# Performance work log

Measured on AMD Instinct MI355X. Metric: run time of the kernel, lower is better.

Reference implementation:

```python
import jax, jax.numpy as jnp
import numpy as np

STRIDE = 1
PADDING = 3
DILATION = 1


def setup_inputs() -> dict:
    key = jax.random.key(0)
    k1, k2 = jax.random.split(key)
    B, C, H, W = 8, 512, 64, 64
    G, K = 8, 7
    Ho, Wo = H // STRIDE, W // STRIDE
    x = jax.random.normal(k1, (B, C, H, W), dtype=jnp.float32)
    weight = jax.random.normal(k2, (B, G, K, K, Ho, Wo), dtype=jnp.float32)
    return {"x": x, "weight": weight}


def reference(x, weight):
    # x: [B, C, H, W]; weight: [B, G, K, K, Ho, Wo]
    B, C, H, W = x.shape
    _, G, K, _, Ho, Wo = weight.shape
    cpg = C // G  # channels per group
    # zero-pad spatial dims (matches CUDA boundary check)
    xp = jnp.pad(x, ((0, 0), (0, 0), (PADDING, PADDING), (PADDING, PADDING)))
    out = jnp.zeros((B, G, cpg, Ho, Wo), dtype=x.dtype)
    for kh in range(K):
        for kw in range(K):
            h0 = kh * DILATION
            w0 = kw * DILATION
            # strided window: input pixel h*stride - pad + kh*dil for each output h
            patch = xp[:, :,
                       h0:h0 + (Ho - 1) * STRIDE + 1:STRIDE,
                       w0:w0 + (Wo - 1) * STRIDE + 1:STRIDE]  # [B, C, Ho, Wo]
            wk = weight[:, :, kh, kw]  # [B, G, Ho, Wo]
            out = out + patch.reshape(B, G, cpg, Ho, Wo) * wk[:, :, None]
    return out.reshape(B, C, Ho, Wo)
```

## Files before the change

kernel.cpp:

```cpp
#include <hip/hip_runtime.h>


#define BB 8
#define CC 512
#define GG 8
#define CPG 64
#define HH 64
#define WW 64
#define HW (HH * WW)
#define KK 7
#define PAD 3

#define TILE_ROWS 16
#define CSPLIT 16
#define CHPC 4
#define LDS_ROWS (TILE_ROWS + KK - 1)
#define LDS_PITCH 72
#define CH_STRIDE (LDS_ROWS * LDS_PITCH)
#define PLANE_QUADS (LDS_ROWS * (LDS_PITCH / 4))
#define TOT_QUADS (CHPC * PLANE_QUADS)
#define NPASS ((TOT_QUADS + 255) / 256)

__global__ __launch_bounds__(256, 4)
void involution_kernel(const float* __restrict__ x,
                       const float* __restrict__ weight,
                       float* __restrict__ out) {
    const int tid = threadIdx.x;
    const int tx = tid & 15;
    const int ty = tid >> 4;

    const int f = blockIdx.x;
    const int xcd = f & 7;
    const int k = f >> 3;
    const int bg = ((k >> 6) << 3) + xcd;
    const int sub = k & 63;
    const int b = bg >> 3;
    const int g = bg & 7;
    const int tile = sub >> 4;
    const int cs = sub & 15;

    const int wo0 = tx << 2;
    const int hbase = tile * TILE_ROWS;
    const int ho = hbase + ty;

    __shared__ float xs[CHPC * CH_STRIDE];

    const float* wq = weight + ((size_t)(b * GG + g) * (KK * KK)) * HW
                    + ho * WW + wo0;

    const size_t cbase = (size_t)(b * CC + g * CPG + cs * CHPC) * HW;
    const float* xg = x + cbase;
    float* og = out + cbase + ho * WW + wo0;

    {
        float4 sv[NPASS];
        int lofs[NPASS];
        bool act[NPASS];
#pragma unroll
        for (int i = 0; i < NPASS; ++i) {
            const int q = tid + i * 256;
            act[i] = (q < TOT_QUADS);
            const int p = q / PLANE_QUADS;
            const int r = q - p * PLANE_QUADS;
            const int sr = r / 18;
            const int sq = r - sr * 18;
            const int xrow = hbase + sr - PAD;
            const int xcol = (sq << 2) - 4;
            const bool ld = act[i]
                         && ((unsigned)xrow < HH) && ((unsigned)xcol < WW);
            float4 v = make_float4(0.f, 0.f, 0.f, 0.f);
            if (ld)
                v = *(const float4*)(xg + (size_t)p * HW + xrow * WW + xcol);
            sv[i] = v;
            lofs[i] = p * CH_STRIDE + sr * LDS_PITCH + (sq << 2);
        }
#pragma unroll
        for (int i = 0; i < NPASS; ++i)
            if (act[i]) *(float4*)(&xs[lofs[i]]) = sv[i];
    }
    __syncthreads();

    float4 acc[CHPC];
#pragma unroll
    for (int ch = 0; ch < CHPC; ++ch)
        acc[ch] = make_float4(0.f, 0.f, 0.f, 0.f);

#pragma unroll
    for (int kh = 0; kh < KK; ++kh) {
        __builtin_amdgcn_sched_barrier(0);
        float4 wk[KK];
#pragma unroll
        for (int j = 0; j < KK; ++j)
            wk[j] = *(const float4*)(wq + (size_t)(kh * KK + j) * HW);

#pragma unroll
        for (int ch = 0; ch < CHPC; ++ch) {
            const float* rowp = &xs[ch * CH_STRIDE + (ty + kh) * LDS_PITCH + wo0];
            const float4 x0 = *(const float4*)(rowp);
            const float4 x1 = *(const float4*)(rowp + 4);
            const float4 x2 = *(const float4*)(rowp + 8);
            const float w1 = x0.y, w2 = x0.z, w3 = x0.w;
            const float w4 = x1.x, w5 = x1.y, w6 = x1.z, w7 = x1.w;
            const float w8 = x2.x, w9 = x2.y, w10 = x2.z;
            float4 a = acc[ch];
            a.x = fmaf(w1, wk[0].x, a.x);  a.y = fmaf(w2, wk[0].y, a.y);
            a.z = fmaf(w3, wk[0].z, a.z);  a.w = fmaf(w4, wk[0].w, a.w);
            a.x = fmaf(w2, wk[1].x, a.x);  a.y = fmaf(w3, wk[1].y, a.y);
            a.z = fmaf(w4, wk[1].z, a.z);  a.w = fmaf(w5, wk[1].w, a.w);
            a.x = fmaf(w3, wk[2].x, a.x);  a.y = fmaf(w4, wk[2].y, a.y);
            a.z = fmaf(w5, wk[2].z, a.z);  a.w = fmaf(w6, wk[2].w, a.w);
            a.x = fmaf(w4, wk[3].x, a.x);  a.y = fmaf(w5, wk[3].y, a.y);
            a.z = fmaf(w6, wk[3].z, a.z);  a.w = fmaf(w7, wk[3].w, a.w);
            a.x = fmaf(w5, wk[4].x, a.x);  a.y = fmaf(w6, wk[4].y, a.y);
            a.z = fmaf(w7, wk[4].z, a.z);  a.w = fmaf(w8, wk[4].w, a.w);
            a.x = fmaf(w6, wk[5].x, a.x);  a.y = fmaf(w7, wk[5].y, a.y);
            a.z = fmaf(w8, wk[5].z, a.z);  a.w = fmaf(w9, wk[5].w, a.w);
            a.x = fmaf(w7, wk[6].x, a.x);  a.y = fmaf(w8, wk[6].y, a.y);
            a.z = fmaf(w9, wk[6].z, a.z);  a.w = fmaf(w10, wk[6].w, a.w);
            acc[ch] = a;
        }
    }

#pragma unroll
    for (int ch = 0; ch < CHPC; ++ch)
        *(float4*)(og + (size_t)ch * HW) = acc[ch];
}

extern "C" void kernel_launch(void* const* d_in, const int* in_sizes, int n_in,
                              void* d_out, int out_size, void* d_ws, size_t ws_size,
                              hipStream_t stream) {
    const float* x = (const float*)d_in[0];
    const float* w = (const float*)d_in[1];
    float* out = (float*)d_out;

    dim3 grid((HH / TILE_ROWS) * CSPLIT * GG * BB);
    dim3 block(256);
    involution_kernel<<<grid, block, 0, stream>>>(x, w, out);
}
```

Before: 195.3 us.

## Double channels per block, transpose LDS layout, double-buffer weight loads

Each block now processes 8 channels instead of 4, halving the number of blocks and doubling reuse of each weight load across channels. The LDS tile is stored in a quarter-transposed layout so each thread reads scalar elements with consecutive lanes hitting consecutive addresses, replacing overlapping float4 reads. Weight rows for the next kh are prefetched into a second register buffer while the current row is computed. The cost is higher register pressure, relaxed occupancy hints (waves_per_eu 2-4), more LDS per block, and more scalar LDS reads and writes.

```diff
diff --git a/kernel.cpp b/kernel.cpp
--- a/kernel.cpp
+++ b/kernel.cpp
@@ -12,16 +12,18 @@
 #define PAD 3
 
 #define TILE_ROWS 16
-#define CSPLIT 16
-#define CHPC 4
+#define CSPLIT 8
+#define CHPC 8
 #define LDS_ROWS (TILE_ROWS + KK - 1)
 #define LDS_PITCH 72
+#define QUARTER 18
 #define CH_STRIDE (LDS_ROWS * LDS_PITCH)
-#define PLANE_QUADS (LDS_ROWS * (LDS_PITCH / 4))
+#define PLANE_QUADS (LDS_ROWS * 18)
 #define TOT_QUADS (CHPC * PLANE_QUADS)
-#define NPASS ((TOT_QUADS + 255) / 256)
+#define NPASS 13
 
-__global__ __launch_bounds__(256, 4)
+__global__ __launch_bounds__(256)
+__attribute__((amdgpu_waves_per_eu(2, 4)))
 void involution_kernel(const float* __restrict__ x,
                        const float* __restrict__ weight,
                        float* __restrict__ out) {
@@ -32,12 +34,12 @@
     const int f = blockIdx.x;
     const int xcd = f & 7;
     const int k = f >> 3;
-    const int bg = ((k >> 6) << 3) + xcd;
-    const int sub = k & 63;
+    const int bg = ((k >> 5) << 3) + xcd;
+    const int sub = k & 31;
     const int b = bg >> 3;
     const int g = bg & 7;
-    const int tile = sub >> 4;
-    const int cs = sub & 15;
+    const int tile = sub >> 3;
+    const int cs = sub & 7;
 
     const int wo0 = tx << 2;
     const int hbase = tile * TILE_ROWS;
@@ -52,31 +54,41 @@
     const float* xg = x + cbase;
     float* og = out + cbase + ho * WW + wo0;
 
-    {
-        float4 sv[NPASS];
-        int lofs[NPASS];
-        bool act[NPASS];
+    float4 sv[NPASS];
+    int lofs[NPASS];
+    bool act[NPASS];
 #pragma unroll
-        for (int i = 0; i < NPASS; ++i) {
-            const int q = tid + i * 256;
-            act[i] = (q < TOT_QUADS);
-            const int p = q / PLANE_QUADS;
-            const int r = q - p * PLANE_QUADS;
-            const int sr = r / 18;
-            const int sq = r - sr * 18;
-            const int xrow = hbase + sr - PAD;
-            const int xcol = (sq << 2) - 4;
-            const bool ld = act[i]
-                         && ((unsigned)xrow < HH) && ((unsigned)xcol < WW);
-            float4 v = make_float4(0.f, 0.f, 0.f, 0.f);
-            if (ld)
-                v = *(const float4*)(xg + (size_t)p * HW + xrow * WW + xcol);
-            sv[i] = v;
-            lofs[i] = p * CH_STRIDE + sr * LDS_PITCH + (sq << 2);
+    for (int i = 0; i < NPASS; ++i) {
+        const int Q = tid + i * 256;
+        act[i] = (Q < TOT_QUADS);
+        const int ch = Q / PLANE_QUADS;
+        const int rem = Q - ch * PLANE_QUADS;
+        const int sr = rem / 18;
+        const int sq = rem - sr * 18;
+        const int xrow = hbase + sr - PAD;
+        const int xcol = (sq << 2) - 4;
+        const bool ld = act[i]
+                     && ((unsigned)xrow < HH) && ((unsigned)xcol < WW);
+        float4 v = make_float4(0.f, 0.f, 0.f, 0.f);
+        if (ld)
+            v = *(const float4*)(xg + (size_t)ch * HW + xrow * WW + xcol);
+        sv[i] = v;
+        lofs[i] = ch * CH_STRIDE + sr * LDS_PITCH + sq;
+    }
+
+    float4 wka[KK], wkb[KK];
+#pragma unroll
+    for (int j = 0; j < KK; ++j)
+        wka[j] = *(const float4*)(wq + (size_t)j * HW);
+
+#pragma unroll
+    for (int i = 0; i < NPASS; ++i) {
+        if (act[i]) {
+            xs[lofs[i]]               = sv[i].x;
+            xs[lofs[i] + QUARTER]     = sv[i].y;
+            xs[lofs[i] + 2 * QUARTER] = sv[i].z;
+            xs[lofs[i] + 3 * QUARTER] = sv[i].w;
         }
-#pragma unroll
-        for (int i = 0; i < NPASS; ++i)
-            if (act[i]) *(float4*)(&xs[lofs[i]]) = sv[i];
     }
     __syncthreads();
 
@@ -85,41 +97,53 @@
     for (int ch = 0; ch < CHPC; ++ch)
         acc[ch] = make_float4(0.f, 0.f, 0.f, 0.f);
 
-#pragma unroll
-    for (int kh = 0; kh < KK; ++kh) {
-        __builtin_amdgcn_sched_barrier(0);
-        float4 wk[KK];
-#pragma unroll
-        for (int j = 0; j < KK; ++j)
-            wk[j] = *(const float4*)(wq + (size_t)(kh * KK + j) * HW);
+#define KH_STEP(KH, WCUR, WNXT, NKH, LN)                                    \
+    {                                                                       \
+        if (LN) {                                                           \
+            _Pragma("unroll")                                               \
+            for (int j = 0; j < KK; ++j)                                    \
+                WNXT[j] = *(const float4*)(wq + (size_t)((NKH) * KK + j) * HW); \
+        }                                                                   \
+        _Pragma("unroll")                                                   \
+        for (int ch = 0; ch < CHPC; ++ch) {                                 \
+            const int b2 = ch * CH_STRIDE + (ty + (KH)) * LDS_PITCH;        \
+            const float v0 = xs[b2 + QUARTER + tx];                         \
+            const float v1 = xs[b2 + 2 * QUARTER + tx];                     \
+            const float v2 = xs[b2 + 3 * QUARTER + tx];                     \
+            const float v3 = xs[b2 + tx + 1];                               \
+            const float v4 = xs[b2 + QUARTER + tx + 1];                     \
+            const float v5 = xs[b2 + 2 * QUARTER + tx + 1];                 \
+            const float v6 = xs[b2 + 3 * QUARTER + tx + 1];                 \
+            const float v7 = xs[b2 + tx + 2];                               \
+            const float v8 = xs[b2 + QUARTER + tx + 2];                     \
+            const float v9 = xs[b2 + 2 * QUARTER + tx + 2];                 \
+            float4 a = acc[ch];                                             \
+            a.x = fmaf(v0, WCUR[0].x, a.x);  a.y = fmaf(v1, WCUR[0].y, a.y); \
+            a.z = fmaf(v2, WCUR[0].z, a.z);  a.w = fmaf(v3, WCUR[0].w, a.w); \
+            a.x = fmaf(v1, WCUR[1].x, a.x);  a.y = fmaf(v2, WCUR[1].y, a.y); \
+            a.z = fmaf(v3, WCUR[1].z, a.z);  a.w = fmaf(v4, WCUR[1].w, a.w); \
+            a.x = fmaf(v2, WCUR[2].x, a.x);  a.y = fmaf(v3, WCUR[2].y, a.y); \
+            a.z = fmaf(v4, WCUR[2].z, a.z);  a.w = fmaf(v5, WCUR[2].w, a.w); \
+            a.x = fmaf(v3, WCUR[3].x, a.x);  a.y = fmaf(v4, WCUR[3].y, a.y); \
+            a.z = fmaf(v5, WCUR[3].z, a.z);  a.w = fmaf(v6, WCUR[3].w, a.w); \
+            a.x = fmaf(v4, WCUR[4].x, a.x);  a.y = fmaf(v5, WCUR[4].y, a.y); \
+            a.z = fmaf(v6, WCUR[4].z, a.z);  a.w = fmaf(v7, WCUR[4].w, a.w); \
+            a.x = fmaf(v5, WCUR[5].x, a.x);  a.y = fmaf(v6, WCUR[5].y, a.y); \
+            a.z = fmaf(v7, WCUR[5].z, a.z);  a.w = fmaf(v8, WCUR[5].w, a.w); \
+            a.x = fmaf(v6, WCUR[6].x, a.x);  a.y = fmaf(v7, WCUR[6].y, a.y); \
+            a.z = fmaf(v8, WCUR[6].z, a.z);  a.w = fmaf(v9, WCUR[6].w, a.w); \
+            acc[ch] = a;                                                    \
+        }                                                                   \
+    }
 
-#pragma unroll
-        for (int ch = 0; ch < CHPC; ++ch) {
-            const float* rowp = &xs[ch * CH_STRIDE + (ty + kh) * LDS_PITCH + wo0];
-            const float4 x0 = *(const float4*)(rowp);
-            const float4 x1 = *(const float4*)(rowp + 4);
-            const float4 x2 = *(const float4*)(rowp + 8);
-            const float w1 = x0.y, w2 = x0.z, w3 = x0.w;
-            const float w4 = x1.x, w5 = x1.y, w6 = x1.z, w7 = x1.w;
-            const float w8 = x2.x, w9 = x2.y, w10 = x2.z;
-            float4 a = acc[ch];
-            a.x = fmaf(w1, wk[0].x, a.x);  a.y = fmaf(w2, wk[0].y, a.y);
-            a.z = fmaf(w3, wk[0].z, a.z);  a.w = fmaf(w4, wk[0].w, a.w);
-            a.x = fmaf(w2, wk[1].x, a.x);  a.y = fmaf(w3, wk[1].y, a.y);
-            a.z = fmaf(w4, wk[1].z, a.z);  a.w = fmaf(w5, wk[1].w, a.w);
-            a.x = fmaf(w3, wk[2].x, a.x);  a.y = fmaf(w4, wk[2].y, a.y);
-            a.z = fmaf(w5, wk[2].z, a.z);  a.w = fmaf(w6, wk[2].w, a.w);
-            a.x = fmaf(w4, wk[3].x, a.x);  a.y = fmaf(w5, wk[3].y, a.y);
-            a.z = fmaf(w6, wk[3].z, a.z);  a.w = fmaf(w7, wk[3].w, a.w);
-            a.x = fmaf(w5, wk[4].x, a.x);  a.y = fmaf(w6, wk[4].y, a.y);
-            a.z = fmaf(w7, wk[4].z, a.z);  a.w = fmaf(w8, wk[4].w, a.w);
-            a.x = fmaf(w6, wk[5].x, a.x);  a.y = fmaf(w7, wk[5].y, a.y);
-            a.z = fmaf(w8, wk[5].z, a.z);  a.w = fmaf(w9, wk[5].w, a.w);
-            a.x = fmaf(w7, wk[6].x, a.x);  a.y = fmaf(w8, wk[6].y, a.y);
-            a.z = fmaf(w9, wk[6].z, a.z);  a.w = fmaf(w10, wk[6].w, a.w);
-            acc[ch] = a;
-        }
-    }
+    KH_STEP(0, wka, wkb, 1, true)
+    KH_STEP(1, wkb, wka, 2, true)
+    KH_STEP(2, wka, wkb, 3, true)
+    KH_STEP(3, wkb, wka, 4, true)
+    KH_STEP(4, wka, wkb, 5, true)
+    KH_STEP(5, wkb, wka, 6, true)
+    KH_STEP(6, wka, wkb, 0, false)
+#undef KH_STEP
 
 #pragma unroll
     for (int ch = 0; ch < CHPC; ++ch)
```

New measurement: 175.8 us. 10.0% less time.
